# Optimization experiments

Measured on AMD Instinct MI355X. Metric: run time of the kernel, lower is better.

The kernel has to match this reference:

```python
import jax, jax.numpy as jnp
import numpy as np

V, E, H = 512, 128, 256
B, S, T = 2048, 32, 48


def setup_inputs() -> dict:
    key = jax.random.key(0)
    ks = jax.random.split(key, 13)
    def p(i, shape):
        return jax.random.normal(ks[i], shape, dtype=jnp.float32) * 0.05
    return {
        "source": jax.random.randint(ks[0], (B, S), 0, V),
        "target_len": T,
        "enc_emb": p(1, (V, E)),
        "enc_Wih": p(2, (4 * H, E)),
        "enc_Whh": p(3, (4 * H, H)),
        "enc_bih": p(4, (4 * H,)),
        "enc_bhh": p(5, (4 * H,)),
        "dec_emb": p(6, (V, E)),
        "dec_Wih": p(7, (4 * H, E)),
        "dec_Whh": p(8, (4 * H, H)),
        "dec_bih": p(9, (4 * H,)),
        "dec_bhh": p(10, (4 * H,)),
        "fc_W": p(11, (V, H)),
        "fc_b": p(12, (V,)),
    }


def lstm_cell(x, h, c, Wih, Whh, bih, bhh):
    # torch gate order: i, f, g, o
    z = x @ Wih.T + h @ Whh.T + (bih + bhh)
    i, f, g, o = jnp.split(z, 4, axis=-1)
    c = jax.nn.sigmoid(f) * c + jax.nn.sigmoid(i) * jnp.tanh(g)
    h = jax.nn.sigmoid(o) * jnp.tanh(c)
    return h, c


def reference(source, target_len, enc_emb, enc_Wih, enc_Whh, enc_bih, enc_bhh,
              dec_emb, dec_Wih, dec_Whh, dec_bih, dec_bhh, fc_W, fc_b):
    Bsz = source.shape[0]
    Hd = enc_Whh.shape[1]
    h0 = jnp.zeros((Bsz, Hd), dtype=enc_emb.dtype)
    c0 = jnp.zeros((Bsz, Hd), dtype=enc_emb.dtype)

    # ---- encoder: embed whole source, scan single-layer LSTM over time ----
    emb_seq = jnp.swapaxes(enc_emb[source], 0, 1)  # [S, B, E]

    def enc_step(carry, x_t):
        h, c = carry
        h, c = lstm_cell(x_t, h, c, enc_Wih, enc_Whh, enc_bih, enc_bhh)
        return (h, c), None

    (h, c), _ = jax.lax.scan(enc_step, (h0, c0), emb_seq)

    sos = jnp.zeros((Bsz,), dtype=jnp.int32)  # char2idx.get('<SOS>', 0) == 0

    def dec_step(carry, _):
        tok, h, c = carry
        x = dec_emb[tok]                         # [B, E]
        h, c = lstm_cell(x, h, c, dec_Wih, dec_Whh, dec_bih, dec_bhh)
        logits = h @ fc_W.T + fc_b               # [B, V]
        nxt = jnp.argmax(logits, axis=-1).astype(jnp.int32)
        return (nxt, h, c), logits

    _, logits = jax.lax.scan(dec_step, (sos, h, c), None, length=target_len)
    return jnp.swapaxes(logits, 0, 1)            # [B, target_len, V]
```

## Files before the change

### kernel.cpp

```cpp
#include <hip/hip_runtime.h>
#include <cmath>

#define S_LEN 32
#define E_DIM 128
#define H_DIM 256
#define V_DIM 512
#define NTILE 18
#define W_TILES 12
#define TILE_SHORTS 8192
#define A_SHORTS 24576
#define ZPITCH 132

typedef _Float16 f16x8v __attribute__((ext_vector_type(8)));
typedef __attribute__((ext_vector_type(4))) float f32x4v;

#define SCALE_S 4096.0f
#define INV_S   2.44140625e-4f

__device__ __forceinline__ float sigf(float x) { return 1.0f / (1.0f + expf(-x)); }

template<int L>
__device__ __forceinline__ unsigned short lvl_f16(float x) {
  _Float16 h1 = (_Float16)x;
  if (L == 1) return __builtin_bit_cast(unsigned short, h1);
  _Float16 h2 = (_Float16)((x - (float)h1) * SCALE_S);
  return __builtin_bit_cast(unsigned short, h2);
}

__global__ void prep_weights(const float* __restrict__ eWih, const float* __restrict__ eWhh,
                             const float* __restrict__ dWih, const float* __restrict__ dWhh,
                             unsigned short* __restrict__ We, unsigned short* __restrict__ Wd,
                             float* __restrict__ h0, float* __restrict__ c,
                             int* __restrict__ tok)
{
  const int b = blockIdx.x;
  if (b >= 192) {
    const int pb = b - 192;
    const int gt = pb * 256 + threadIdx.x;
    float4 z = make_float4(0.f, 0.f, 0.f, 0.f);
    float4* p0 = (float4*)h0;
    float4* pc = (float4*)c;
    for (int i = gt; i < 131072; i += 16384) { p0[i] = z; pc[i] = z; }
    if (gt < 2048) tok[gt] = 0;
    return;
  }
  const int j    = b % W_TILES;
  const int rest = b / W_TILES;
  const int nb   = rest & 7;
  const int set  = rest >> 3;
  const float* Wih = set ? dWih : eWih;
  const float* Whh = set ? dWhh : eWhh;
  unsigned short* dst = (set ? Wd : We) + ((size_t)nb * W_TILES + j) * TILE_SHORTS;
  const int lvl = (j < 6) ? 1 : 2;
  const int jj  = (j < 6) ? j : j - 6;

  for (int cpos = threadIdx.x; cpos < 1024; cpos += 256) {
    int fi = cpos >> 6, l = cpos & 63;
    int kh = fi >> 3, wc = (fi >> 2) & 1, g = fi & 3;
    int n  = g * H_DIM + nb * 32 + wc * 16 + (l & 15);
    int kk = jj * 64 + kh * 32 + (l >> 4) * 8;
    unsigned short o8[8];
    #pragma unroll
    for (int e = 0; e < 8; ++e) {
      int k = kk + e;
      float v = (k < E_DIM) ? Wih[(size_t)n * E_DIM + k]
                            : Whh[(size_t)n * H_DIM + (k - E_DIM)];
      o8[e] = (lvl == 1) ? lvl_f16<1>(v) : lvl_f16<2>(v);
    }
    uint4 pk;
    pk.x = (unsigned)o8[0] | ((unsigned)o8[1] << 16);
    pk.y = (unsigned)o8[2] | ((unsigned)o8[3] << 16);
    pk.z = (unsigned)o8[4] | ((unsigned)o8[5] << 16);
    pk.w = (unsigned)o8[6] | ((unsigned)o8[7] << 16);
    *(uint4*)&dst[(size_t)cpos * 8] = pk;
  }
}

__device__ __forceinline__ void stage_A12(unsigned short* Ax1, unsigned short* Ax2,
                                          const float* __restrict__ esrc,
                                          const float* __restrict__ hsrc,
                                          int arow, int q4) {
  const int rowblk = arow >> 4;
  const int rlo    = arow & 15;
  #pragma unroll
  for (int j = 0; j < 24; ++j) {
    int k0, kA;
    const float* src;
    if (j < 8) { k0 = q4 * 4 + 16 * j; kA = k0; src = esrc + k0; }
    else       { k0 = q4 * 4 + 16 * (j - 8); kA = E_DIM + k0; src = hsrc + k0; }
    float4 v = *(const float4*)src;
    _Float16 a1x = (_Float16)v.x, a1y = (_Float16)v.y,
             a1z = (_Float16)v.z, a1w = (_Float16)v.w;
    _Float16 a2x = (_Float16)((v.x - (float)a1x) * SCALE_S);
    _Float16 a2y = (_Float16)((v.y - (float)a1y) * SCALE_S);
    _Float16 a2z = (_Float16)((v.z - (float)a1z) * SCALE_S);
    _Float16 a2w = (_Float16)((v.w - (float)a1w) * SCALE_S);
    int lane_w = rlo + ((kA & 31) >> 3) * 16;
    int idx = (((kA >> 5) * 4 + rowblk) * 64 + lane_w) * 8 + (kA & 7);
    uint2 p1, p2;
    p1.x = (unsigned)__builtin_bit_cast(unsigned short, a1x)
         | ((unsigned)__builtin_bit_cast(unsigned short, a1y) << 16);
    p1.y = (unsigned)__builtin_bit_cast(unsigned short, a1z)
         | ((unsigned)__builtin_bit_cast(unsigned short, a1w) << 16);
    p2.x = (unsigned)__builtin_bit_cast(unsigned short, a2x)
         | ((unsigned)__builtin_bit_cast(unsigned short, a2y) << 16);
    p2.y = (unsigned)__builtin_bit_cast(unsigned short, a2z)
         | ((unsigned)__builtin_bit_cast(unsigned short, a2w) << 16);
    *(uint2*)&Ax1[idx] = p1;
    *(uint2*)&Ax2[idx] = p2;
  }
}

__launch_bounds__(256)
__global__ void lstm_mfma_kernel(const float* __restrict__ emb,
                                 const int* __restrict__ idx_src, int idx_stride, int idx_off,
                                 const unsigned short* __restrict__ Wf,
                                 const float* __restrict__ bih, const float* __restrict__ bhh,
                                 const float* __restrict__ h_in,
                                 float* __restrict__ h_out, float* __restrict__ c)
{
  __shared__ __align__(16) unsigned short Ax1[A_SHORTS];
  __shared__ __align__(16) unsigned short Ax2[A_SHORTS];

  const int tid  = threadIdx.x;
  const int lane = tid & 63;
  const int m0 = blockIdx.x * 64;
  const int nb = blockIdx.y;
  const int nc0 = nb * 32;

  const int arow = tid >> 2;
  const int q4   = tid & 3;
  const int token = idx_src[(size_t)(m0 + arow) * idx_stride + idx_off];
  const float* esrc = emb + (size_t)token * E_DIM;
  const float* hsrc = h_in + (size_t)(m0 + arow) * H_DIM;

  const int wm = (tid >> 6) & 1;
  const int wc = tid >> 7;
  const int lr = tid & 15;
  const int l4 = lane >> 4;

  const unsigned short* wbase = Wf + (size_t)nb * (W_TILES * TILE_SHORTS)
                                   + (size_t)(wc * 4) * 512 + (size_t)lane * 8;

  f32x4v accA[2][4], accB[2][4];
  #pragma unroll
  for (int mf = 0; mf < 2; ++mf)
    #pragma unroll
    for (int g = 0; g < 4; ++g) {
      accA[mf][g] = (f32x4v){0.f, 0.f, 0.f, 0.f};
      accB[mf][g] = (f32x4v){0.f, 0.f, 0.f, 0.f};
    }

  uint4 pA[8], pB[8], pC[8];

#define LOADT(J, P)                                                            \
  {                                                                            \
    const unsigned short* bsrc =                                               \
        wbase + (size_t)(((J) < W_TILES) ? (J) : (J) - W_TILES) * TILE_SHORTS; \
    _Pragma("unroll")                                                          \
    for (int f = 0; f < 4; ++f) {                                              \
      P[f]     = *(const uint4*)(bsrc + (size_t)f * 512);                      \
      P[4 + f] = *(const uint4*)(bsrc + (size_t)(8 + f) * 512);                \
    }                                                                          \
  }

#define MFMAT(J, P, ACC, AXB)                                                  \
  {                                                                            \
    const int ks0 = ((J) % 6) * 2;                                             \
    _Pragma("unroll")                                                          \
    for (int kh = 0; kh < 2; ++kh) {                                           \
      f16x8v af0 = *(const f16x8v*)&AXB[((ks0 + kh) * 4 + wm * 2) * 512 + lane * 8];      \
      f16x8v af1 = *(const f16x8v*)&AXB[((ks0 + kh) * 4 + wm * 2 + 1) * 512 + lane * 8];  \
      _Pragma("unroll")                                                        \
      for (int g = 0; g < 4; ++g) {                                            \
        f16x8v bfr = __builtin_bit_cast(f16x8v, P[kh * 4 + g]);                \
        ACC[0][g] = __builtin_amdgcn_mfma_f32_16x16x32_f16(af0, bfr, ACC[0][g], 0, 0, 0); \
        ACC[1][g] = __builtin_amdgcn_mfma_f32_16x16x32_f16(af1, bfr, ACC[1][g], 0, 0, 0); \
      }                                                                        \
    }                                                                          \
  }

  LOADT(0, pA); LOADT(1, pB);

  stage_A12(Ax1, Ax2, esrc, hsrc, arow, q4);
  asm volatile("s_waitcnt lgkmcnt(0)" ::: "memory");
  __builtin_amdgcn_s_barrier();

  LOADT(2, pC);  MFMAT(0, pA, accA, Ax1);
  LOADT(3, pA);  MFMAT(1, pB, accA, Ax1);
  LOADT(4, pB);  MFMAT(2, pC, accA, Ax1);
  LOADT(5, pC);  MFMAT(3, pA, accA, Ax1);
  LOADT(6, pA);  MFMAT(4, pB, accA, Ax1);
  LOADT(7, pB);  MFMAT(5, pC, accA, Ax1);
  LOADT(8, pC);  MFMAT(6, pA, accB, Ax1);
  LOADT(9, pA);  MFMAT(7, pB, accB, Ax1);
  LOADT(10, pB); MFMAT(8, pC, accB, Ax1);
  LOADT(11, pC); MFMAT(9, pA, accB, Ax1);
  LOADT(12, pA); MFMAT(10, pB, accB, Ax1);
  LOADT(13, pB); MFMAT(11, pC, accB, Ax1);
  LOADT(14, pC); MFMAT(12, pA, accB, Ax2);
  LOADT(15, pA); MFMAT(13, pB, accB, Ax2);
  LOADT(16, pB); MFMAT(14, pC, accB, Ax2);
  LOADT(17, pC);

  const int er  = tid >> 2;
  const int ec4 = (tid & 3) * 2;
  const float* cp0 = c + (size_t)(m0 + er) * H_DIM + nc0 + ec4 * 4;
  float4 cold0 = *(const float4*)(cp0);
  float4 cold1 = *(const float4*)(cp0 + 4);

  MFMAT(15, pA, accB, Ax2);
  MFMAT(16, pB, accB, Ax2);
  MFMAT(17, pC, accB, Ax2);

#undef LOADT
#undef MFMAT

  float bs[4];
  #pragma unroll
  for (int g = 0; g < 4; ++g)
    bs[g] = bih[g * H_DIM + nc0 + wc * 16 + lr] + bhh[g * H_DIM + nc0 + wc * 16 + lr];

  float* zb = (float*)Ax1;
  asm volatile("s_waitcnt lgkmcnt(0)" ::: "memory");
  __builtin_amdgcn_s_barrier();

  #pragma unroll
  for (int mf = 0; mf < 2; ++mf)
    #pragma unroll
    for (int r = 0; r < 4; ++r) {
      int row_l = wm * 32 + mf * 16 + l4 * 4 + r;
      int base = row_l * ZPITCH + (wc * 16 + lr) * 4;
      #pragma unroll
      for (int g = 0; g < 4; ++g)
        zb[base + g] = fmaf(accB[mf][g][r], INV_S, accA[mf][g][r]) + bs[g];
    }

  asm volatile("s_waitcnt lgkmcnt(0)" ::: "memory");
  __builtin_amdgcn_s_barrier();

  {
    float* hp = h_out + (size_t)(m0 + er) * H_DIM + nc0 + ec4 * 4;
    float* cpw = (float*)cp0;
    #pragma unroll
    for (int s = 0; s < 2; ++s) {
      int c4 = ec4 + s;
      float4 cold = s ? cold1 : cold0;
      float cov[4] = {cold.x, cold.y, cold.z, cold.w};
      float cnv[4], hnv[4];
      #pragma unroll
      for (int j = 0; j < 4; ++j) {
        float4 zq = *(const float4*)&zb[er * ZPITCH + c4 * 16 + j * 4];
        float zi = zq.x, zf = zq.y, zg = zq.z, zo = zq.w;
        float cn = sigf(zf) * cov[j] + sigf(zi) * tanhf(zg);
        cnv[j] = cn;
        hnv[j] = sigf(zo) * tanhf(cn);
      }
      *(float4*)(cpw + s * 4) = make_float4(cnv[0], cnv[1], cnv[2], cnv[3]);
      *(float4*)(hp + s * 4)  = make_float4(hnv[0], hnv[1], hnv[2], hnv[3]);
    }
  }
}

__launch_bounds__(256)
__global__ void declog_kernel(const float* __restrict__ h,
                              const float* __restrict__ fcW,
                              const float* __restrict__ fcb,
                              float* __restrict__ out,
                              int* __restrict__ tok,
                              int t, int T)
{
  __shared__ float bv[8][256];
  __shared__ int   bi[8][256];

  const int tid  = threadIdx.x;
  const int lane = tid & 63;
  const int wv   = tid >> 6;
  const int r0   = blockIdx.x * 8;
  const int c0   = tid * 2;

  const float* hb  = h + (size_t)r0 * H_DIM;
  const float* w0p = fcW + (size_t)c0 * H_DIM;
  const float* w1p = w0p + H_DIM;

  float acc[8][2] = {};

  #pragma unroll 1
  for (int k0 = 0; k0 < H_DIM; k0 += 16) {
    float4 b0[4], b1[4];
    #pragma unroll
    for (int q = 0; q < 4; ++q) {
      b0[q] = *(const float4*)(w0p + k0 + q * 4);
      b1[q] = *(const float4*)(w1p + k0 + q * 4);
    }
    #pragma unroll
    for (int q = 0; q < 4; ++q) {
      #pragma unroll
      for (int r = 0; r < 8; ++r) {
        float4 a = *(const float4*)(hb + (size_t)r * H_DIM + k0 + q * 4);
        acc[r][0] = fmaf(a.x, b0[q].x, acc[r][0]);
        acc[r][0] = fmaf(a.y, b0[q].y, acc[r][0]);
        acc[r][0] = fmaf(a.z, b0[q].z, acc[r][0]);
        acc[r][0] = fmaf(a.w, b0[q].w, acc[r][0]);
        acc[r][1] = fmaf(a.x, b1[q].x, acc[r][1]);
        acc[r][1] = fmaf(a.y, b1[q].y, acc[r][1]);
        acc[r][1] = fmaf(a.z, b1[q].z, acc[r][1]);
        acc[r][1] = fmaf(a.w, b1[q].w, acc[r][1]);
      }
    }
  }

  const float fb0 = fcb[c0];
  const float fb1 = fcb[c0 + 1];
  #pragma unroll
  for (int r = 0; r < 8; ++r) {
    float z0 = acc[r][0] + fb0;
    float z1 = acc[r][1] + fb1;
    *(float2*)(out + (size_t)(r0 + r) * T * V_DIM + (size_t)t * V_DIM + c0)
        = make_float2(z0, z1);
    float v = z0; int ix = c0;
    if (z1 > v) { v = z1; ix = c0 + 1; }
    bv[r][tid] = v;
    bi[r][tid] = ix;
  }
  __syncthreads();

  #pragma unroll
  for (int rr = 0; rr < 2; ++rr) {
    int r = wv * 2 + rr;
    float best = bv[r][lane];
    int   bidx = bi[r][lane];
    #pragma unroll
    for (int s = 1; s < 4; ++s) {
      float ov = bv[r][lane + 64 * s];
      int   oi = bi[r][lane + 64 * s];
      if (ov > best || (ov == best && oi < bidx)) { best = ov; bidx = oi; }
    }
    #pragma unroll
    for (int off = 32; off; off >>= 1) {
      float ov = __shfl_xor(best, off);
      int   oi = __shfl_xor(bidx, off);
      if (ov > best || (ov == best && oi < bidx)) { best = ov; bidx = oi; }
    }
    if (lane == 0) tok[r0 + r] = bidx;
  }
}

extern "C" void kernel_launch(void* const* d_in, const int* in_sizes, int n_in,
                              void* d_out, int out_size, void* d_ws, size_t ws_size,
                              hipStream_t stream) {
  const int*   source  = (const int*)d_in[0];
  const float* enc_emb = (const float*)d_in[2];
  const float* enc_Wih = (const float*)d_in[3];
  const float* enc_Whh = (const float*)d_in[4];
  const float* enc_bih = (const float*)d_in[5];
  const float* enc_bhh = (const float*)d_in[6];
  const float* dec_emb = (const float*)d_in[7];
  const float* dec_Wih = (const float*)d_in[8];
  const float* dec_Whh = (const float*)d_in[9];
  const float* dec_bih = (const float*)d_in[10];
  const float* dec_bhh = (const float*)d_in[11];
  const float* fc_W    = (const float*)d_in[12];
  const float* fc_b    = (const float*)d_in[13];
  float* out = (float*)d_out;

  const int B = in_sizes[0] / S_LEN;
  const int T = out_size / (B * V_DIM);

  const size_t BH = (size_t)B * H_DIM;
  const size_t WFSZ = (size_t)8 * W_TILES * TILE_SHORTS;
  float* h0  = (float*)d_ws;
  float* h1  = h0 + BH;
  float* c   = h1 + BH;
  int*   tok = (int*)(c + BH);
  unsigned short* We = (unsigned short*)(tok + B);
  unsigned short* Wd = We + WFSZ;

  prep_weights<<<dim3(192 + 64), dim3(256), 0, stream>>>(
      enc_Wih, enc_Whh, dec_Wih, dec_Whh, We, Wd, h0, c, tok);

  dim3 blk(256);
  dim3 g_lstm(B / 64, H_DIM / 32);
  dim3 g_declog(B / 8);

  const float* hin = h0;
  float* hout = h1;

  for (int s = 0; s < S_LEN; ++s) {
    lstm_mfma_kernel<<<g_lstm, blk, 0, stream>>>(
        enc_emb, source, S_LEN, s, We, enc_bih, enc_bhh, hin, hout, c);
    const float* tmp = hout; hout = (float*)hin; hin = tmp;
  }

  for (int t = 0; t < T; ++t) {
    lstm_mfma_kernel<<<g_lstm, blk, 0, stream>>>(
        dec_emb, tok, 1, 0, Wd, dec_bih, dec_bhh, hin, hout, c);
    const float* tmp = hout; hout = (float*)hin; hin = tmp;
    declog_kernel<<<g_declog, blk, 0, stream>>>(hin, fc_W, fc_b, out, tok, t, T);
  }
}
```

Before: 2.020 ms.

## Halve LSTM block row tile to 32 and deepen weight prefetch to four buffers

Each LSTM block now handles 32 batch rows instead of 64, which doubles the grid to 512 blocks and halves the shared-memory A staging and per-wave accumulators. The aim is to fill more CUs and raise occupancy (launch bounds now request 2 blocks per SM) in a small-batch, latency-bound recurrent step. The weight tile pipeline goes from three to four register buffers so loads run further ahead. In exchange, each weight tile is read from memory by twice as many blocks, and each MFMA B fragment is reused only once instead of twice.

```diff
diff --git a/kernel.cpp b/kernel.cpp
--- a/kernel.cpp
+++ b/kernel.cpp
@@ -8,7 +8,7 @@
 #define NTILE 18
 #define W_TILES 12
 #define TILE_SHORTS 8192
-#define A_SHORTS 24576
+#define A_SHORTS 12288
 #define ZPITCH 132
 
 typedef _Float16 f16x8v __attribute__((ext_vector_type(8)));
@@ -79,15 +79,15 @@
 __device__ __forceinline__ void stage_A12(unsigned short* Ax1, unsigned short* Ax2,
                                           const float* __restrict__ esrc,
                                           const float* __restrict__ hsrc,
-                                          int arow, int q4) {
+                                          int arow, int q8) {
   const int rowblk = arow >> 4;
   const int rlo    = arow & 15;
   #pragma unroll
-  for (int j = 0; j < 24; ++j) {
+  for (int j = 0; j < 12; ++j) {
     int k0, kA;
     const float* src;
-    if (j < 8) { k0 = q4 * 4 + 16 * j; kA = k0; src = esrc + k0; }
-    else       { k0 = q4 * 4 + 16 * (j - 8); kA = E_DIM + k0; src = hsrc + k0; }
+    if (j < 4) { kA = q8 * 4 + 32 * j;            src = esrc + kA; }
+    else       { k0 = q8 * 4 + 32 * (j - 4); kA = E_DIM + k0; src = hsrc + k0; }
     float4 v = *(const float4*)src;
     _Float16 a1x = (_Float16)v.x, a1y = (_Float16)v.y,
              a1z = (_Float16)v.z, a1w = (_Float16)v.w;
@@ -96,7 +96,7 @@
     _Float16 a2z = (_Float16)((v.z - (float)a1z) * SCALE_S);
     _Float16 a2w = (_Float16)((v.w - (float)a1w) * SCALE_S);
     int lane_w = rlo + ((kA & 31) >> 3) * 16;
-    int idx = (((kA >> 5) * 4 + rowblk) * 64 + lane_w) * 8 + (kA & 7);
+    int idx = (((kA >> 5) * 2 + rowblk) * 64 + lane_w) * 8 + (kA & 7);
     uint2 p1, p2;
     p1.x = (unsigned)__builtin_bit_cast(unsigned short, a1x)
          | ((unsigned)__builtin_bit_cast(unsigned short, a1y) << 16);
@@ -111,7 +111,7 @@
   }
 }
 
-__launch_bounds__(256)
+__launch_bounds__(256, 2)
 __global__ void lstm_mfma_kernel(const float* __restrict__ emb,
                                  const int* __restrict__ idx_src, int idx_stride, int idx_off,
                                  const unsigned short* __restrict__ Wf,
@@ -124,12 +124,12 @@
 
   const int tid  = threadIdx.x;
   const int lane = tid & 63;
-  const int m0 = blockIdx.x * 64;
+  const int m0 = blockIdx.x * 32;
   const int nb = blockIdx.y;
   const int nc0 = nb * 32;
 
-  const int arow = tid >> 2;
-  const int q4   = tid & 3;
+  const int arow = tid >> 3;
+  const int q8   = tid & 7;
   const int token = idx_src[(size_t)(m0 + arow) * idx_stride + idx_off];
   const float* esrc = emb + (size_t)token * E_DIM;
   const float* hsrc = h_in + (size_t)(m0 + arow) * H_DIM;
@@ -142,16 +142,14 @@
   const unsigned short* wbase = Wf + (size_t)nb * (W_TILES * TILE_SHORTS)
                                    + (size_t)(wc * 4) * 512 + (size_t)lane * 8;
 
-  f32x4v accA[2][4], accB[2][4];
-  #pragma unroll
-  for (int mf = 0; mf < 2; ++mf)
-    #pragma unroll
-    for (int g = 0; g < 4; ++g) {
-      accA[mf][g] = (f32x4v){0.f, 0.f, 0.f, 0.f};
-      accB[mf][g] = (f32x4v){0.f, 0.f, 0.f, 0.f};
-    }
-
-  uint4 pA[8], pB[8], pC[8];
+  f32x4v accA[4], accB[4];
+  #pragma unroll
+  for (int g = 0; g < 4; ++g) {
+    accA[g] = (f32x4v){0.f, 0.f, 0.f, 0.f};
+    accB[g] = (f32x4v){0.f, 0.f, 0.f, 0.f};
+  }
+
+  uint4 pA[8], pB[8], pC[8], pD[8];
 
 #define LOADT(J, P)                                                            \
   {                                                                            \
@@ -169,49 +167,45 @@
     const int ks0 = ((J) % 6) * 2;                                             \
     _Pragma("unroll")                                                          \
     for (int kh = 0; kh < 2; ++kh) {                                           \
-      f16x8v af0 = *(const f16x8v*)&AXB[((ks0 + kh) * 4 + wm * 2) * 512 + lane * 8];      \
-      f16x8v af1 = *(const f16x8v*)&AXB[((ks0 + kh) * 4 + wm * 2 + 1) * 512 + lane * 8];  \
+      f16x8v af = *(const f16x8v*)&AXB[((ks0 + kh) * 2 + wm) * 512 + lane * 8]; \
       _Pragma("unroll")                                                        \
       for (int g = 0; g < 4; ++g) {                                            \
         f16x8v bfr = __builtin_bit_cast(f16x8v, P[kh * 4 + g]);                \
-        ACC[0][g] = __builtin_amdgcn_mfma_f32_16x16x32_f16(af0, bfr, ACC[0][g], 0, 0, 0); \
-        ACC[1][g] = __builtin_amdgcn_mfma_f32_16x16x32_f16(af1, bfr, ACC[1][g], 0, 0, 0); \
+        ACC[g] = __builtin_amdgcn_mfma_f32_16x16x32_f16(af, bfr, ACC[g], 0, 0, 0); \
       }                                                                        \
     }                                                                          \
   }
 
-  LOADT(0, pA); LOADT(1, pB);
-
-  stage_A12(Ax1, Ax2, esrc, hsrc, arow, q4);
+  LOADT(0, pA); LOADT(1, pB); LOADT(2, pC);
+
+  stage_A12(Ax1, Ax2, esrc, hsrc, arow, q8);
   asm volatile("s_waitcnt lgkmcnt(0)" ::: "memory");
   __builtin_amdgcn_s_barrier();
 
-  LOADT(2, pC);  MFMAT(0, pA, accA, Ax1);
-  LOADT(3, pA);  MFMAT(1, pB, accA, Ax1);
-  LOADT(4, pB);  MFMAT(2, pC, accA, Ax1);
-  LOADT(5, pC);  MFMAT(3, pA, accA, Ax1);
-  LOADT(6, pA);  MFMAT(4, pB, accA, Ax1);
-  LOADT(7, pB);  MFMAT(5, pC, accA, Ax1);
-  LOADT(8, pC);  MFMAT(6, pA, accB, Ax1);
-  LOADT(9, pA);  MFMAT(7, pB, accB, Ax1);
-  LOADT(10, pB); MFMAT(8, pC, accB, Ax1);
-  LOADT(11, pC); MFMAT(9, pA, accB, Ax1);
-  LOADT(12, pA); MFMAT(10, pB, accB, Ax1);
-  LOADT(13, pB); MFMAT(11, pC, accB, Ax1);
-  LOADT(14, pC); MFMAT(12, pA, accB, Ax2);
-  LOADT(15, pA); MFMAT(13, pB, accB, Ax2);
-  LOADT(16, pB); MFMAT(14, pC, accB, Ax2);
-  LOADT(17, pC);
-
-  const int er  = tid >> 2;
-  const int ec4 = (tid & 3) * 2;
-  const float* cp0 = c + (size_t)(m0 + er) * H_DIM + nc0 + ec4 * 4;
-  float4 cold0 = *(const float4*)(cp0);
-  float4 cold1 = *(const float4*)(cp0 + 4);
-
-  MFMAT(15, pA, accB, Ax2);
-  MFMAT(16, pB, accB, Ax2);
-  MFMAT(17, pC, accB, Ax2);
+  LOADT(3, pD);  MFMAT(0, pA, accA, Ax1);
+  LOADT(4, pA);  MFMAT(1, pB, accA, Ax1);
+  LOADT(5, pB);  MFMAT(2, pC, accA, Ax1);
+  LOADT(6, pC);  MFMAT(3, pD, accA, Ax1);
+  LOADT(7, pD);  MFMAT(4, pA, accA, Ax1);
+  LOADT(8, pA);  MFMAT(5, pB, accA, Ax1);
+  LOADT(9, pB);  MFMAT(6, pC, accB, Ax1);
+  LOADT(10, pC); MFMAT(7, pD, accB, Ax1);
+  LOADT(11, pD); MFMAT(8, pA, accB, Ax1);
+  LOADT(12, pA); MFMAT(9, pB, accB, Ax1);
+  LOADT(13, pB); MFMAT(10, pC, accB, Ax1);
+  LOADT(14, pC); MFMAT(11, pD, accB, Ax1);
+  LOADT(15, pD); MFMAT(12, pA, accB, Ax2);
+  LOADT(16, pA); MFMAT(13, pB, accB, Ax2);
+  LOADT(17, pB); MFMAT(14, pC, accB, Ax2);
+
+  const int er = tid >> 3;
+  const int ec = tid & 7;
+  const float* cp0 = c + (size_t)(m0 + er) * H_DIM + nc0 + ec * 4;
+  float4 cold = *(const float4*)(cp0);
+
+  MFMAT(15, pD, accB, Ax2);
+  MFMAT(16, pA, accB, Ax2);
+  MFMAT(17, pB, accB, Ax2);
 
 #undef LOADT
 #undef MFMAT
@@ -226,39 +220,32 @@
   __builtin_amdgcn_s_barrier();
 
   #pragma unroll
-  for (int mf = 0; mf < 2; ++mf)
-    #pragma unroll
-    for (int r = 0; r < 4; ++r) {
-      int row_l = wm * 32 + mf * 16 + l4 * 4 + r;
-      int base = row_l * ZPITCH + (wc * 16 + lr) * 4;
-      #pragma unroll
-      for (int g = 0; g < 4; ++g)
-        zb[base + g] = fmaf(accB[mf][g][r], INV_S, accA[mf][g][r]) + bs[g];
-    }
+  for (int r = 0; r < 4; ++r) {
+    int row_l = wm * 16 + l4 * 4 + r;
+    int base = row_l * ZPITCH + (wc * 16 + lr) * 4;
+    #pragma unroll
+    for (int g = 0; g < 4; ++g)
+      zb[base + g] = fmaf(accB[g][r], INV_S, accA[g][r]) + bs[g];
+  }
 
   asm volatile("s_waitcnt lgkmcnt(0)" ::: "memory");
   __builtin_amdgcn_s_barrier();
 
   {
-    float* hp = h_out + (size_t)(m0 + er) * H_DIM + nc0 + ec4 * 4;
+    float* hp  = h_out + (size_t)(m0 + er) * H_DIM + nc0 + ec * 4;
     float* cpw = (float*)cp0;
-    #pragma unroll
-    for (int s = 0; s < 2; ++s) {
-      int c4 = ec4 + s;
-      float4 cold = s ? cold1 : cold0;
-      float cov[4] = {cold.x, cold.y, cold.z, cold.w};
-      float cnv[4], hnv[4];
-      #pragma unroll
-      for (int j = 0; j < 4; ++j) {
-        float4 zq = *(const float4*)&zb[er * ZPITCH + c4 * 16 + j * 4];
-        float zi = zq.x, zf = zq.y, zg = zq.z, zo = zq.w;
-        float cn = sigf(zf) * cov[j] + sigf(zi) * tanhf(zg);
-        cnv[j] = cn;
-        hnv[j] = sigf(zo) * tanhf(cn);
-      }
-      *(float4*)(cpw + s * 4) = make_float4(cnv[0], cnv[1], cnv[2], cnv[3]);
-      *(float4*)(hp + s * 4)  = make_float4(hnv[0], hnv[1], hnv[2], hnv[3]);
-    }
+    float cov[4] = {cold.x, cold.y, cold.z, cold.w};
+    float cnv[4], hnv[4];
+    #pragma unroll
+    for (int cc = 0; cc < 4; ++cc) {
+      float4 zq = *(const float4*)&zb[er * ZPITCH + (ec * 4 + cc) * 4];
+      float zi = zq.x, zf = zq.y, zg = zq.z, zo = zq.w;
+      float cn = sigf(zf) * cov[cc] + sigf(zi) * tanhf(zg);
+      cnv[cc] = cn;
+      hnv[cc] = sigf(zo) * tanhf(cn);
+    }
+    *(float4*)cpw = make_float4(cnv[0], cnv[1], cnv[2], cnv[3]);
+    *(float4*)hp  = make_float4(hnv[0], hnv[1], hnv[2], hnv[3]);
   }
 }
 
@@ -380,7 +367,7 @@
       enc_Wih, enc_Whh, dec_Wih, dec_Whh, We, Wd, h0, c, tok);
 
   dim3 blk(256);
-  dim3 g_lstm(B / 64, H_DIM / 32);
+  dim3 g_lstm(B / 32, H_DIM / 32);
   dim3 g_declog(B / 8);
 
   const float* hin = h0;
```

Measured after the change: 1.980 ms. 2.0% less time.
